# Kernel optimization log

Measured on AMD Instinct MI355X. Metric: run time of the kernel, lower is better.

Reference implementation:

```python
import jax, jax.numpy as jnp
import numpy as np

N, E, F_IN, DIM, HEADS = 16384, 262144, 128, 64, 4
HID = DIM * HEADS  # 256
NEG = 0.2


def _lin(k, fan_in, fan_out):
    kw, kb = jax.random.split(k)
    s = 1.0 / np.sqrt(fan_in)
    return (jax.random.uniform(kw, (fan_in, fan_out), jnp.float32, -s, s),
            jax.random.uniform(kb, (fan_out,), jnp.float32, -s, s))


def setup_inputs() -> dict:
    key = jax.random.key(0)
    ks = jax.random.split(key, 20)
    x = jax.random.normal(ks[0], (N, F_IN), jnp.float32)
    edge_index = jax.random.randint(ks[1], (2, E), 0, N, jnp.int32)
    Win, b_in = _lin(ks[2], F_IN, DIM)
    Wskip, bskip = _lin(ks[3], DIM, HID)
    # conv1: in=DIM, out per head=DIM, heads=HEADS, concat -> HID
    Wl1, _ = _lin(ks[4], DIM, HID)
    Wr1, _ = _lin(ks[5], DIM, HID)
    att1 = jax.random.normal(ks[6], (HEADS, DIM), jnp.float32) * 0.1
    b1 = jnp.zeros((HID,), jnp.float32)
    # conv2: in=HID, out=HID, heads=1, concat=False
    Wl2, _ = _lin(ks[7], HID, HID)
    Wr2, _ = _lin(ks[8], HID, HID)
    att2 = jax.random.normal(ks[9], (1, HID), jnp.float32) * 0.1
    b2 = jnp.zeros((HID,), jnp.float32)
    # conv3: in=HID, out=HID, heads=1, concat=False
    Wl3, _ = _lin(ks[10], HID, HID)
    Wr3, _ = _lin(ks[11], HID, HID)
    att3 = jax.random.normal(ks[12], (1, HID), jnp.float32) * 0.1
    b3 = jnp.zeros((HID,), jnp.float32)
    Wm1, bm1 = _lin(ks[13], HID, DIM)
    Wm2, bm2 = _lin(ks[14], DIM, DIM)
    Wm3, bm3 = _lin(ks[15], DIM, 1)
    return dict(x=x, edge_index=edge_index, Win=Win, b_in=b_in,
                Wskip=Wskip, bskip=bskip,
                Wl1=Wl1, Wr1=Wr1, att1=att1, b1=b1,
                Wl2=Wl2, Wr2=Wr2, att2=att2, b2=b2,
                Wl3=Wl3, Wr3=Wr3, att3=att3, b3=b3,
                Wm1=Wm1, bm1=bm1, Wm2=Wm2, bm2=bm2, Wm3=Wm3, bm3=bm3)


def gatv2(x, src, dst, Wl, Wr, att, b, concat):
    # PyG GATv2Conv: x_l = lin_l(x)[src], x_r = lin_r(x)[dst]
    n = x.shape[0]
    H, D = att.shape
    xl = (x @ Wl).reshape(n, H, D)
    xr = (x @ Wr).reshape(n, H, D)
    e = jax.nn.leaky_relu(xl[src] + xr[dst], NEG)          # [E, H, D]
    logits = jnp.einsum('ehd,hd->eh', e, att)              # [E, H]
    m = jax.ops.segment_max(logits, dst, num_segments=n)   # per-dst softmax
    alpha = jnp.exp(logits - m[dst])
    denom = jax.ops.segment_sum(alpha, dst, num_segments=n)
    alpha = alpha / denom[dst]
    out = jax.ops.segment_sum(alpha[:, :, None] * xl[src], dst, num_segments=n)
    out = out.reshape(n, H * D) if concat else out.mean(axis=1)
    return out + b


def reference(x, edge_index, Win, b_in, Wskip, bskip,
              Wl1, Wr1, att1, b1, Wl2, Wr2, att2, b2,
              Wl3, Wr3, att3, b3, Wm1, bm1, Wm2, bm2, Wm3, bm3):
    n = x.shape[0]
    # add self loops (GATv2Conv default add_self_loops=True)
    loop = jnp.arange(n, dtype=edge_index.dtype)
    src = jnp.concatenate([edge_index[0], loop])
    dst = jnp.concatenate([edge_index[1], loop])

    h = jax.nn.relu(x @ Win + b_in)                         # [N, DIM]
    out1 = jax.nn.relu(gatv2(h, src, dst, Wl1, Wr1, att1, b1, True))
    out1 = out1 + (h @ Wskip + bskip)                       # [N, HID]
    out2 = jax.nn.relu(gatv2(out1, src, dst, Wl2, Wr2, att2, b2, False))
    out2 = out2 + out1
    out3 = jax.nn.relu(gatv2(out2, src, dst, Wl3, Wr3, att3, b3, False))
    out3 = out3 + out2
    out = jax.nn.relu(out3 @ Wm1 + bm1)
    out = jax.nn.relu(out @ Wm2 + bm2)
    out = out @ Wm3 + bm3                                   # [N, 1]
    return out.reshape(-1)
```

## Files before the change

### kernel.cpp

```cpp
#include <hip/hip_runtime.h>
#include <cstdint>
#include <cstddef>

#define N_NODES 16384
#define E_EDGES 262144
#define FIN     128
#define DIM     64
#define HID     256
#define NEG     0.2f

typedef _Float16 h8 __attribute__((ext_vector_type(8)));
typedef _Float16 h4 __attribute__((ext_vector_type(4)));
typedef _Float16 h2 __attribute__((ext_vector_type(2)));
typedef float    f32x4 __attribute__((ext_vector_type(4)));
typedef float    f32x2 __attribute__((ext_vector_type(2)));

__global__ __launch_bounds__(256) void zero_cnt_kernel(int4* __restrict__ cnt) {
    cnt[blockIdx.x * 256 + threadIdx.x] = make_int4(0, 0, 0, 0);
}

__global__ __launch_bounds__(256) void hist_kernel(const int* __restrict__ dst,
                                                   int* __restrict__ cnt) {
    int i = blockIdx.x * 256 + threadIdx.x;
    if (i < E_EDGES) atomicAdd(&cnt[dst[i]], 1);
}

__global__ __launch_bounds__(256) void csr_scan_kernel(const int* __restrict__ cnt,
                                                       int* __restrict__ offs,
                                                       int* __restrict__ cursor) {
    __shared__ int wsum[4];
    int tid = threadIdx.x, lane = tid & 63, w = tid >> 6;
    int base = tid * 64;
    const int4* c4 = (const int4*)(cnt + base);
    int4 v[16];
    int s = 0;
#pragma unroll
    for (int i = 0; i < 16; ++i) {
        v[i] = c4[i];
        s += v[i].x + v[i].y + v[i].z + v[i].w;
    }
    int scan = s;
#pragma unroll
    for (int off = 1; off < 64; off <<= 1) {
        int t = __shfl_up(scan, off);
        if (lane >= off) scan += t;
    }
    if (lane == 63) wsum[w] = scan;
    __syncthreads();
    int wbase = 0;
#pragma unroll
    for (int i = 0; i < 4; ++i) if (i < w) wbase += wsum[i];
    int run = wbase + (scan - s);
#pragma unroll
    for (int i = 0; i < 16; ++i) {
        int4 o;
        o.x = run;
        o.y = o.x + v[i].x;
        o.z = o.y + v[i].y;
        o.w = o.z + v[i].z;
        *(int4*)(offs + base + 4 * i) = o;
        *(int4*)(cursor + base + 4 * i) = o;
        run = o.w + v[i].w;
    }
    if (tid == 255) offs[N_NODES] = run;
}

__global__ __launch_bounds__(256) void scatter_kernel(const int* __restrict__ src,
                                                      const int* __restrict__ dst,
                                                      int* __restrict__ cursor,
                                                      int* __restrict__ esrc) {
    int i = blockIdx.x * 256 + threadIdx.x;
    if (i < E_EDGES) {
        int p = atomicAdd(&cursor[dst[i]], 1);
        esrc[p] = src[i];
    }
}

struct PackJob { const float* W; _Float16* dst; int Ksrc, Nsrc, NT, colOff; };
struct PackJobs { PackJob j[10]; };

__global__ __launch_bounds__(256) void pack_all_kernel(PackJobs jobs) {
    PackJob jb = jobs.j[blockIdx.y];
    int i = blockIdx.x * 256 + threadIdx.x;
    if (i < jb.Ksrc * jb.Nsrc) {
        int k = i / jb.Nsrc, n = i % jb.Nsrc;
        jb.dst[((size_t)(k >> 3) * jb.NT + jb.colOff + n) * 8 + (k & 7)] = (_Float16)jb.W[i];
    }
}

template<int K, bool RELU, bool O16, bool IN32>
__global__ __launch_bounds__(64) void mfma_n64_kernel(const void* __restrict__ Av,
                                                      const _Float16* __restrict__ Wp,
                                                      const float* __restrict__ bias,
                                                      void* __restrict__ outv) {
    int lane = threadIdx.x;
    int rowBase = blockIdx.x * 64;
    int l15 = lane & 15, l4 = lane >> 4;

    f32x4 acc[4][4] = {};
#pragma unroll
    for (int ks = 0; ks < K / 32; ++ks) {
        h8 af[4], bf[4];
#pragma unroll
        for (int mi = 0; mi < 4; ++mi) {
            if constexpr (IN32) {
                const float* ap = (const float*)Av + (size_t)(rowBase + mi * 16 + l15) * K + ks * 32 + l4 * 8;
                float4 a0 = *(const float4*)ap;
                float4 a1 = *(const float4*)(ap + 4);
                h8 v;
                v[0] = (_Float16)a0.x; v[1] = (_Float16)a0.y;
                v[2] = (_Float16)a0.z; v[3] = (_Float16)a0.w;
                v[4] = (_Float16)a1.x; v[5] = (_Float16)a1.y;
                v[6] = (_Float16)a1.z; v[7] = (_Float16)a1.w;
                af[mi] = v;
            } else {
                af[mi] = *(const h8*)((const _Float16*)Av + (size_t)(rowBase + mi * 16 + l15) * K + ks * 32 + l4 * 8);
            }
        }
#pragma unroll
        for (int ni = 0; ni < 4; ++ni)
            bf[ni] = *(const h8*)(Wp + ((size_t)(ks * 4 + l4) * 64 + ni * 16 + l15) * 8);
#pragma unroll
        for (int mi = 0; mi < 4; ++mi)
#pragma unroll
            for (int ni = 0; ni < 4; ++ni)
                acc[mi][ni] = __builtin_amdgcn_mfma_f32_16x16x32_f16(af[mi], bf[ni], acc[mi][ni], 0, 0, 0);
    }
#pragma unroll
    for (int mi = 0; mi < 4; ++mi)
#pragma unroll
        for (int ni = 0; ni < 4; ++ni) {
            int c = ni * 16 + l15;
            float bv = bias[c];
#pragma unroll
            for (int q = 0; q < 4; ++q) {
                int r = rowBase + mi * 16 + l4 * 4 + q;
                float v = acc[mi][ni][q] + bv;
                if (RELU) v = fmaxf(v, 0.f);
                if constexpr (O16) ((_Float16*)outv)[(size_t)r * 64 + c] = (_Float16)v;
                else               ((float*)outv)[(size_t)r * 64 + c] = v;
            }
        }
}

template<int K>
__global__ __launch_bounds__(256) void mfma_gemm_kernel(const _Float16* __restrict__ A,
                                                        const _Float16* __restrict__ Wp,
                                                        int NT,
                                                        _Float16* __restrict__ o16a,
                                                        _Float16* __restrict__ o16b,
                                                        float* __restrict__ o32,
                                                        const float* __restrict__ bias) {
    int tid = threadIdx.x;
    int lane = tid & 63, wid = tid >> 6;
    int wm = wid >> 1, wn = wid & 1;
    int rowBase = blockIdx.x * 128 + wm * 64;
    int colBase = blockIdx.y * 128 + wn * 64;
    int l15 = lane & 15, l4 = lane >> 4;

    f32x4 acc[4][4] = {};
#pragma unroll
    for (int ks = 0; ks < K / 32; ++ks) {
        h8 af[4], bf[4];
#pragma unroll
        for (int mi = 0; mi < 4; ++mi)
            af[mi] = *(const h8*)(A + (size_t)(rowBase + mi * 16 + l15) * K + ks * 32 + l4 * 8);
#pragma unroll
        for (int ni = 0; ni < 4; ++ni)
            bf[ni] = *(const h8*)(Wp + ((size_t)(ks * 4 + l4) * NT + colBase + ni * 16 + l15) * 8);
#pragma unroll
        for (int mi = 0; mi < 4; ++mi)
#pragma unroll
            for (int ni = 0; ni < 4; ++ni)
                acc[mi][ni] = __builtin_amdgcn_mfma_f32_16x16x32_f16(af[mi], bf[ni], acc[mi][ni], 0, 0, 0);
    }

    int seg = colBase >> 8;
    int cbase = colBase & 255;
    if (o32 != nullptr && seg == 2) {
#pragma unroll
        for (int mi = 0; mi < 4; ++mi)
#pragma unroll
            for (int ni = 0; ni < 4; ++ni) {
                int c = cbase + ni * 16 + l15;
                float bv = bias[c];
#pragma unroll
                for (int q = 0; q < 4; ++q) {
                    int r = rowBase + mi * 16 + l4 * 4 + q;
                    o32[(size_t)r * 256 + c] = acc[mi][ni][q] + bv;
                }
            }
    } else {
        _Float16* o = (seg == 0) ? o16a : o16b;
#pragma unroll
        for (int mi = 0; mi < 4; ++mi)
#pragma unroll
            for (int ni = 0; ni < 4; ++ni) {
                int c = cbase + ni * 16 + l15;
#pragma unroll
                for (int q = 0; q < 4; ++q) {
                    int r = rowBase + mi * 16 + l4 * 4 + q;
                    o[(size_t)r * 256 + c] = (_Float16)acc[mi][ni][q];
                }
            }
    }
}

template<int H, int OMODE>
__global__ __launch_bounds__(256) void gat_agg_kernel(const _Float16* __restrict__ xl,
                                                      const _Float16* __restrict__ xr,
                                                      const float* __restrict__ att,
                                                      const float* __restrict__ bias,
                                                      const float* __restrict__ resid,
                                                      const int* __restrict__ offs,
                                                      const int* __restrict__ esrc,
                                                      float* __restrict__ out,
                                                      _Float16* __restrict__ out16) {
    int tid = threadIdx.x;
    int wid = tid >> 6;
    int lane = tid & 63;
    int node = blockIdx.x * 4 + wid;
    int g  = lane >> 4;
    int li = lane & 15;

    h2 xrv[8];
    {
        const h8* xp = (const h8*)(xr + ((size_t)node << 8) + (li << 4));
        h8 a0 = xp[0], a1 = xp[1];
#pragma unroll
        for (int i = 0; i < 4; ++i) { xrv[i][0] = a0[2 * i]; xrv[i][1] = a0[2 * i + 1]; }
#pragma unroll
        for (int i = 0; i < 4; ++i) { xrv[4 + i][0] = a1[2 * i]; xrv[4 + i][1] = a1[2 * i + 1]; }
    }
    h2 attv[8];
    {
        const float4* ap = (const float4*)(att + (li << 4));
#pragma unroll
        for (int i = 0; i < 4; ++i) {
            float4 a = ap[i];
            attv[2 * i][0] = (_Float16)a.x; attv[2 * i][1] = (_Float16)a.y;
            attv[2 * i + 1][0] = (_Float16)a.z; attv[2 * i + 1][1] = (_Float16)a.w;
        }
    }
    const h2 negc = { (_Float16)NEG, (_Float16)NEG };

    float m = -1e30f, s = 0.f;
    f32x2 acc2[8];
#pragma unroll
    for (int i = 0; i < 8; ++i) acc2[i] = (f32x2){0.f, 0.f};

    int e0 = offs[node];
    int total = offs[node + 1] - e0 + 1;

    auto gather = [&](int srcn, h2* hv) {
        const h8* xp = (const h8*)(xl + ((size_t)srcn << 8) + (li << 4));
        h8 a0 = xp[0], a1 = xp[1];
#pragma unroll
        for (int i = 0; i < 4; ++i) { hv[i][0] = a0[2 * i]; hv[i][1] = a0[2 * i + 1]; }
#pragma unroll
        for (int i = 0; i < 4; ++i) { hv[4 + i][0] = a1[2 * i]; hv[4 + i][1] = a1[2 * i + 1]; }
    };
    auto logit = [&](const h2* hv) -> float {
        float part = 0.f;
#pragma unroll
        for (int i = 0; i < 8; ++i) {
            h2 sum = hv[i] + xrv[i];
            h2 lr = __builtin_elementwise_max(sum, sum * negc);
            part = __builtin_amdgcn_fdot2(lr, attv[i], part, false);
        }
        part += __shfl_xor(part, 1);
        part += __shfl_xor(part, 2);
        if constexpr (H == 1) {
            part += __shfl_xor(part, 4);
            part += __shfl_xor(part, 8);
        }
        return part;
    };

    int vi = g;
    for (; vi + 4 < total; vi += 8) {
        int sA = (vi == 0) ? node : esrc[e0 + vi - 1];
        int sB = esrc[e0 + vi + 3];
        h2 hA[8], hB[8];
        gather(sA, hA);
        gather(sB, hB);
        float lpA = logit(hA);
        float lpB = logit(hB);
        float mn = fmaxf(m, fmaxf(lpA, lpB));
        float c  = __expf(m - mn);
        float pA = __expf(lpA - mn);
        float pB = __expf(lpB - mn);
        s = s * c + pA + pB;
#pragma unroll
        for (int i = 0; i < 8; ++i) {
            f32x2 t = acc2[i] * c;
            t[0] = fmaf(pA, (float)hA[i][0], t[0]);
            t[1] = fmaf(pA, (float)hA[i][1], t[1]);
            t[0] = fmaf(pB, (float)hB[i][0], t[0]);
            t[1] = fmaf(pB, (float)hB[i][1], t[1]);
            acc2[i] = t;
        }
        m = mn;
    }
    for (; vi < total; vi += 4) {
        int srcn = (vi == 0) ? node : esrc[e0 + vi - 1];
        h2 hA[8];
        gather(srcn, hA);
        float lp = logit(hA);
        float mn = fmaxf(m, lp);
        float c = __expf(m - mn);
        float p = __expf(lp - mn);
        s = s * c + p;
#pragma unroll
        for (int i = 0; i < 8; ++i) {
            f32x2 t = acc2[i] * c;
            t[0] = fmaf(p, (float)hA[i][0], t[0]);
            t[1] = fmaf(p, (float)hA[i][1], t[1]);
            acc2[i] = t;
        }
        m = mn;
    }

#pragma unroll
    for (int mask = 16; mask <= 32; mask <<= 1) {
        float m2 = __shfl_xor(m, mask);
        float s2 = __shfl_xor(s, mask);
        float M = fmaxf(m, m2);
        float c1 = __expf(m - M);
        float c2 = __expf(m2 - M);
        s = s * c1 + s2 * c2;
#pragma unroll
        for (int i = 0; i < 8; ++i) {
            float ax = __shfl_xor(acc2[i][0], mask);
            float ay = __shfl_xor(acc2[i][1], mask);
            acc2[i][0] = acc2[i][0] * c1 + ax * c2;
            acc2[i][1] = acc2[i][1] * c1 + ay * c2;
        }
        m = M;
    }

    float inv = 1.f / s;
    float a0, a1v, a2, a3;
    if (g == 0)      { a0 = acc2[0][0]; a1v = acc2[0][1]; a2 = acc2[1][0]; a3 = acc2[1][1]; }
    else if (g == 1) { a0 = acc2[2][0]; a1v = acc2[2][1]; a2 = acc2[3][0]; a3 = acc2[3][1]; }
    else if (g == 2) { a0 = acc2[4][0]; a1v = acc2[4][1]; a2 = acc2[5][0]; a3 = acc2[5][1]; }
    else             { a0 = acc2[6][0]; a1v = acc2[6][1]; a2 = acc2[7][0]; a3 = acc2[7][1]; }
    int dbase = (li << 4) + (g << 2);
    float4 bv = *(const float4*)(bias + dbase);
    float4 rv = *(const float4*)(resid + ((size_t)node << 8) + dbase);
    float o0 = fmaxf(a0 * inv + bv.x, 0.f) + rv.x;
    float o1 = fmaxf(a1v * inv + bv.y, 0.f) + rv.y;
    float o2 = fmaxf(a2 * inv + bv.z, 0.f) + rv.z;
    float o3 = fmaxf(a3 * inv + bv.w, 0.f) + rv.w;
    if constexpr (OMODE != 2) {
        float4 ov = make_float4(o0, o1, o2, o3);
        *(float4*)(out + ((size_t)node << 8) + dbase) = ov;
    }
    if constexpr (OMODE != 0) {
        h4 hv;
        hv[0] = (_Float16)o0; hv[1] = (_Float16)o1;
        hv[2] = (_Float16)o2; hv[3] = (_Float16)o3;
        *(h4*)(out16 + ((size_t)node << 8) + dbase) = hv;
    }
}

__global__ __launch_bounds__(64) void mlp_head_kernel(const _Float16* __restrict__ A,
                                                      const _Float16* __restrict__ Wm1p,
                                                      const float* __restrict__ bm1,
                                                      const _Float16* __restrict__ Wm2p,
                                                      const float* __restrict__ bm2,
                                                      const float* __restrict__ Wm3,
                                                      const float* __restrict__ bm3,
                                                      float* __restrict__ out) {
    __shared__ _Float16 t1s[64][72];
    int lane = threadIdx.x;
    int rowBase = blockIdx.x * 64;
    int l15 = lane & 15, l4 = lane >> 4;

    f32x4 acc[4][4] = {};
#pragma unroll
    for (int ks = 0; ks < 8; ++ks) {
        h8 af[4], bf[4];
#pragma unroll
        for (int mi = 0; mi < 4; ++mi)
            af[mi] = *(const h8*)(A + (size_t)(rowBase + mi * 16 + l15) * 256 + ks * 32 + l4 * 8);
#pragma unroll
        for (int ni = 0; ni < 4; ++ni)
            bf[ni] = *(const h8*)(Wm1p + ((size_t)(ks * 4 + l4) * 64 + ni * 16 + l15) * 8);
#pragma unroll
        for (int mi = 0; mi < 4; ++mi)
#pragma unroll
            for (int ni = 0; ni < 4; ++ni)
                acc[mi][ni] = __builtin_amdgcn_mfma_f32_16x16x32_f16(af[mi], bf[ni], acc[mi][ni], 0, 0, 0);
    }
#pragma unroll
    for (int mi = 0; mi < 4; ++mi)
#pragma unroll
        for (int ni = 0; ni < 4; ++ni) {
            int c = ni * 16 + l15;
            float bv = bm1[c];
#pragma unroll
            for (int q = 0; q < 4; ++q)
                t1s[mi * 16 + l4 * 4 + q][c] = (_Float16)fmaxf(acc[mi][ni][q] + bv, 0.f);
        }

    f32x4 acc2[4][4] = {};
#pragma unroll
    for (int ks = 0; ks < 2; ++ks) {
        h8 af[4], bf[4];
#pragma unroll
        for (int mi = 0; mi < 4; ++mi)
            af[mi] = *(const h8*)&t1s[mi * 16 + l15][ks * 32 + l4 * 8];
#pragma unroll
        for (int ni = 0; ni < 4; ++ni)
            bf[ni] = *(const h8*)(Wm2p + ((size_t)(ks * 4 + l4) * 64 + ni * 16 + l15) * 8);
#pragma unroll
        for (int mi = 0; mi < 4; ++mi)
#pragma unroll
            for (int ni = 0; ni < 4; ++ni)
                acc2[mi][ni] = __builtin_amdgcn_mfma_f32_16x16x32_f16(af[mi], bf[ni], acc2[mi][ni], 0, 0, 0);
    }

    float b3 = bm3[0];
    float b2v[4], w3v[4];
#pragma unroll
    for (int ni = 0; ni < 4; ++ni) {
        b2v[ni] = bm2[ni * 16 + l15];
        w3v[ni] = Wm3[ni * 16 + l15];
    }
#pragma unroll
    for (int mi = 0; mi < 4; ++mi)
#pragma unroll
        for (int q = 0; q < 4; ++q) {
            float part = 0.f;
#pragma unroll
            for (int ni = 0; ni < 4; ++ni)
                part += fmaxf(acc2[mi][ni][q] + b2v[ni], 0.f) * w3v[ni];
            part += __shfl_xor(part, 1);
            part += __shfl_xor(part, 2);
            part += __shfl_xor(part, 4);
            part += __shfl_xor(part, 8);
            if (l15 == 0)
                out[rowBase + mi * 16 + l4 * 4 + q] = part + b3;
        }
}

extern "C" void kernel_launch(void* const* d_in, const int* in_sizes, int n_in,
                              void* d_out, int out_size, void* d_ws, size_t ws_size,
                              hipStream_t stream) {
    const float* x     = (const float*)d_in[0];
    const int*   ei    = (const int*)d_in[1];
    const float* Win   = (const float*)d_in[2];
    const float* b_in  = (const float*)d_in[3];
    const float* Wskip = (const float*)d_in[4];
    const float* bskip = (const float*)d_in[5];
    const float* Wl1   = (const float*)d_in[6];
    const float* Wr1   = (const float*)d_in[7];
    const float* att1  = (const float*)d_in[8];
    const float* b1    = (const float*)d_in[9];
    const float* Wl2   = (const float*)d_in[10];
    const float* Wr2   = (const float*)d_in[11];
    const float* att2  = (const float*)d_in[12];
    const float* b2    = (const float*)d_in[13];
    const float* Wl3   = (const float*)d_in[14];
    const float* Wr3   = (const float*)d_in[15];
    const float* att3  = (const float*)d_in[16];
    const float* b3    = (const float*)d_in[17];
    const float* Wm1   = (const float*)d_in[18];
    const float* bm1   = (const float*)d_in[19];
    const float* Wm2   = (const float*)d_in[20];
    const float* bm2   = (const float*)d_in[21];
    const float* Wm3   = (const float*)d_in[22];
    const float* bm3   = (const float*)d_in[23];

    char* p = (char*)d_ws;
    auto alloc = [&](size_t bytes) { char* r = p; p += (bytes + 255) & ~(size_t)255; return r; };
    const size_t NN = N_NODES;
    float*    skip = (float*)alloc(NN * 256 * 4);
    float*    out1 = (float*)alloc(NN * 256 * 4);
    _Float16* o116 = (_Float16*)alloc(NN * 256 * 2);
    _Float16* o216 = (_Float16*)alloc(NN * 256 * 2);
    _Float16* o316 = o116;
    _Float16* h16  = (_Float16*)alloc(NN * 64 * 2);
    _Float16* xl16 = (_Float16*)alloc(NN * 256 * 2);
    _Float16* xr16 = (_Float16*)alloc(NN * 256 * 2);
    _Float16* Wp1  = (_Float16*)alloc((size_t)64 * 768 * 2);
    _Float16* Wp2  = (_Float16*)alloc((size_t)256 * 512 * 2);
    _Float16* Wp3  = (_Float16*)alloc((size_t)256 * 512 * 2);
    _Float16* Winp = (_Float16*)alloc((size_t)128 * 64 * 2);
    _Float16* Wm1p = (_Float16*)alloc((size_t)256 * 64 * 2);
    _Float16* Wm2p = (_Float16*)alloc((size_t)64 * 64 * 2);
    int* cnt    = (int*)alloc(N_NODES * 4);
    int* offs   = (int*)alloc((N_NODES + 1) * 4);
    int* cursor = (int*)alloc(N_NODES * 4);
    int* esrc   = (int*)alloc(E_EDGES * 4);

    const int* src = ei;
    const int* dst = ei + E_EDGES;

    zero_cnt_kernel<<<N_NODES / 1024, 256, 0, stream>>>((int4*)cnt);
    hist_kernel<<<E_EDGES / 256, 256, 0, stream>>>(dst, cnt);
    csr_scan_kernel<<<1, 256, 0, stream>>>(cnt, offs, cursor);
    scatter_kernel<<<E_EDGES / 256, 256, 0, stream>>>(src, dst, cursor, esrc);

    PackJobs jobs = {{
        { Wl1,   Wp1,  64,  256, 768, 0   },
        { Wr1,   Wp1,  64,  256, 768, 256 },
        { Wskip, Wp1,  64,  256, 768, 512 },
        { Wl2,   Wp2,  256, 256, 512, 0   },
        { Wr2,   Wp2,  256, 256, 512, 256 },
        { Wl3,   Wp3,  256, 256, 512, 0   },
        { Wr3,   Wp3,  256, 256, 512, 256 },
        { Win,   Winp, 128, 64,  64,  0   },
        { Wm1,   Wm1p, 256, 64,  64,  0   },
        { Wm2,   Wm2p, 64,  64,  64,  0   },
    }};
    pack_all_kernel<<<dim3(256, 10), 256, 0, stream>>>(jobs);

    mfma_n64_kernel<128, true, true, true><<<N_NODES / 64, 64, 0, stream>>>(x, Winp, b_in, h16);

    mfma_gemm_kernel<64><<<dim3(128, 6), 256, 0, stream>>>(h16, Wp1, 768, xl16, xr16, skip, bskip);
    gat_agg_kernel<4, 1><<<N_NODES / 4, 256, 0, stream>>>(xl16, xr16, att1, b1, skip, offs, esrc, out1, o116);

    mfma_gemm_kernel<256><<<dim3(128, 4), 256, 0, stream>>>(o116, Wp2, 512, xl16, xr16, nullptr, nullptr);
    gat_agg_kernel<1, 1><<<N_NODES / 4, 256, 0, stream>>>(xl16, xr16, att2, b2, out1, offs, esrc, skip , o216);

    mfma_gemm_kernel<256><<<dim3(128, 4), 256, 0, stream>>>(o216, Wp3, 512, xl16, xr16, nullptr, nullptr);
    gat_agg_kernel<1, 2><<<N_NODES / 4, 256, 0, stream>>>(xl16, xr16, att3, b3, skip , offs, esrc, nullptr, o316);

    mlp_head_kernel<<<N_NODES / 64, 64, 0, stream>>>(o316, Wm1p, bm1, Wm2p, bm2, Wm3, bm3, (float*)d_out);
}
```

Baseline: 198.7 us.

## Fold count zeroing into pack kernel, unroll GAT gather 4-wide, split MLP head across waves

Removes the separate zero_cnt launch by adding an extra grid row to the weight-pack kernel that clears the histogram counts. The GAT aggregation loop now processes four neighbours per iteration instead of two, giving more outstanding gathers for memory-level parallelism. The bias and residual loads are hoisted ahead of the loop so their latency overlaps it. The MLP head now uses 256-thread blocks with each wave handling 16 rows, which lowers register use per wave and raises occupancy, at the cost of more register pressure in the aggregation kernel.

Result: slower. 210.3 us (+5.8%).

```diff
diff --git a/kernel.cpp b/kernel.cpp
--- a/kernel.cpp
+++ b/kernel.cpp
@@ -14,10 +14,6 @@
 typedef _Float16 h2 __attribute__((ext_vector_type(2)));
 typedef float    f32x4 __attribute__((ext_vector_type(4)));
 typedef float    f32x2 __attribute__((ext_vector_type(2)));
-
-__global__ __launch_bounds__(256) void zero_cnt_kernel(int4* __restrict__ cnt) {
-    cnt[blockIdx.x * 256 + threadIdx.x] = make_int4(0, 0, 0, 0);
-}
 
 __global__ __launch_bounds__(256) void hist_kernel(const int* __restrict__ dst,
                                                    int* __restrict__ cnt) {
@@ -79,9 +75,13 @@
 struct PackJob { const float* W; _Float16* dst; int Ksrc, Nsrc, NT, colOff; };
 struct PackJobs { PackJob j[10]; };
 
-__global__ __launch_bounds__(256) void pack_all_kernel(PackJobs jobs) {
+__global__ __launch_bounds__(256) void pack_all_kernel(PackJobs jobs, int* __restrict__ cnt) {
+    int i = blockIdx.x * 256 + threadIdx.x;
+    if (blockIdx.y == 10) {
+        if (i < N_NODES) cnt[i] = 0;
+        return;
+    }
     PackJob jb = jobs.j[blockIdx.y];
-    int i = blockIdx.x * 256 + threadIdx.x;
     if (i < jb.Ksrc * jb.Nsrc) {
         int k = i / jb.Nsrc, n = i % jb.Nsrc;
         jb.dst[((size_t)(k >> 3) * jb.NT + jb.colOff + n) * 8 + (k & 7)] = (_Float16)jb.W[i];
@@ -244,6 +244,10 @@
     }
     const h2 negc = { (_Float16)NEG, (_Float16)NEG };
 
+    int dbase = (li << 4) + (g << 2);
+    float4 bv = *(const float4*)(bias + dbase);
+    float4 rv = *(const float4*)(resid + ((size_t)node << 8) + dbase);
+
     float m = -1e30f, s = 0.f;
     f32x2 acc2[8];
 #pragma unroll
@@ -278,19 +282,27 @@
     };
 
     int vi = g;
-    for (; vi + 4 < total; vi += 8) {
+    for (; vi + 12 < total; vi += 16) {
         int sA = (vi == 0) ? node : esrc[e0 + vi - 1];
         int sB = esrc[e0 + vi + 3];
-        h2 hA[8], hB[8];
+        int sC = esrc[e0 + vi + 7];
+        int sD = esrc[e0 + vi + 11];
+        h2 hA[8], hB[8], hC[8], hD[8];
         gather(sA, hA);
         gather(sB, hB);
+        gather(sC, hC);
+        gather(sD, hD);
         float lpA = logit(hA);
         float lpB = logit(hB);
-        float mn = fmaxf(m, fmaxf(lpA, lpB));
+        float lpC = logit(hC);
+        float lpD = logit(hD);
+        float mn = fmaxf(m, fmaxf(fmaxf(lpA, lpB), fmaxf(lpC, lpD)));
         float c  = __expf(m - mn);
         float pA = __expf(lpA - mn);
         float pB = __expf(lpB - mn);
-        s = s * c + pA + pB;
+        float pC = __expf(lpC - mn);
+        float pD = __expf(lpD - mn);
+        s = s * c + ((pA + pB) + (pC + pD));
 #pragma unroll
         for (int i = 0; i < 8; ++i) {
             f32x2 t = acc2[i] * c;
@@ -298,6 +310,10 @@
             t[1] = fmaf(pA, (float)hA[i][1], t[1]);
             t[0] = fmaf(pB, (float)hB[i][0], t[0]);
             t[1] = fmaf(pB, (float)hB[i][1], t[1]);
+            t[0] = fmaf(pC, (float)hC[i][0], t[0]);
+            t[1] = fmaf(pC, (float)hC[i][1], t[1]);
+            t[0] = fmaf(pD, (float)hD[i][0], t[0]);
+            t[1] = fmaf(pD, (float)hD[i][1], t[1]);
             acc2[i] = t;
         }
         m = mn;
@@ -345,9 +361,6 @@
     else if (g == 1) { a0 = acc2[2][0]; a1v = acc2[2][1]; a2 = acc2[3][0]; a3 = acc2[3][1]; }
     else if (g == 2) { a0 = acc2[4][0]; a1v = acc2[4][1]; a2 = acc2[5][0]; a3 = acc2[5][1]; }
     else             { a0 = acc2[6][0]; a1v = acc2[6][1]; a2 = acc2[7][0]; a3 = acc2[7][1]; }
-    int dbase = (li << 4) + (g << 2);
-    float4 bv = *(const float4*)(bias + dbase);
-    float4 rv = *(const float4*)(resid + ((size_t)node << 8) + dbase);
     float o0 = fmaxf(a0 * inv + bv.x, 0.f) + rv.x;
     float o1 = fmaxf(a1v * inv + bv.y, 0.f) + rv.y;
     float o2 = fmaxf(a2 * inv + bv.z, 0.f) + rv.z;
@@ -364,61 +377,52 @@
     }
 }
 
-__global__ __launch_bounds__(64) void mlp_head_kernel(const _Float16* __restrict__ A,
-                                                      const _Float16* __restrict__ Wm1p,
-                                                      const float* __restrict__ bm1,
-                                                      const _Float16* __restrict__ Wm2p,
-                                                      const float* __restrict__ bm2,
-                                                      const float* __restrict__ Wm3,
-                                                      const float* __restrict__ bm3,
-                                                      float* __restrict__ out) {
-    __shared__ _Float16 t1s[64][72];
-    int lane = threadIdx.x;
-    int rowBase = blockIdx.x * 64;
+__global__ __launch_bounds__(256) void mlp_head_kernel(const _Float16* __restrict__ A,
+                                                       const _Float16* __restrict__ Wm1p,
+                                                       const float* __restrict__ bm1,
+                                                       const _Float16* __restrict__ Wm2p,
+                                                       const float* __restrict__ bm2,
+                                                       const float* __restrict__ Wm3,
+                                                       const float* __restrict__ bm3,
+                                                       float* __restrict__ out) {
+    __shared__ _Float16 t1s[4][16][72];
+    int tid = threadIdx.x;
+    int lane = tid & 63, wid = tid >> 6;
+    int rowBase = blockIdx.x * 64 + wid * 16;
     int l15 = lane & 15, l4 = lane >> 4;
 
-    f32x4 acc[4][4] = {};
+    f32x4 acc[4] = {};
 #pragma unroll
     for (int ks = 0; ks < 8; ++ks) {
-        h8 af[4], bf[4];
-#pragma unroll
-        for (int mi = 0; mi < 4; ++mi)
-            af[mi] = *(const h8*)(A + (size_t)(rowBase + mi * 16 + l15) * 256 + ks * 32 + l4 * 8);
+        h8 af = *(const h8*)(A + (size_t)(rowBase + l15) * 256 + ks * 32 + l4 * 8);
+        h8 bf[4];
 #pragma unroll
         for (int ni = 0; ni < 4; ++ni)
             bf[ni] = *(const h8*)(Wm1p + ((size_t)(ks * 4 + l4) * 64 + ni * 16 + l15) * 8);
 #pragma unroll
-        for (int mi = 0; mi < 4; ++mi)
-#pragma unroll
-            for (int ni = 0; ni < 4; ++ni)
-                acc[mi][ni] = __builtin_amdgcn_mfma_f32_16x16x32_f16(af[mi], bf[ni], acc[mi][ni], 0, 0, 0);
-    }
-#pragma unroll
-    for (int mi = 0; mi < 4; ++mi)
-#pragma unroll
-        for (int ni = 0; ni < 4; ++ni) {
-            int c = ni * 16 + l15;
-            float bv = bm1[c];
-#pragma unroll
-            for (int q = 0; q < 4; ++q)
-                t1s[mi * 16 + l4 * 4 + q][c] = (_Float16)fmaxf(acc[mi][ni][q] + bv, 0.f);
-        }
-
-    f32x4 acc2[4][4] = {};
+        for (int ni = 0; ni < 4; ++ni)
+            acc[ni] = __builtin_amdgcn_mfma_f32_16x16x32_f16(af, bf[ni], acc[ni], 0, 0, 0);
+    }
+#pragma unroll
+    for (int ni = 0; ni < 4; ++ni) {
+        int c = ni * 16 + l15;
+        float bv = bm1[c];
+#pragma unroll
+        for (int q = 0; q < 4; ++q)
+            t1s[wid][l4 * 4 + q][c] = (_Float16)fmaxf(acc[ni][q] + bv, 0.f);
+    }
+
+    f32x4 acc2[4] = {};
 #pragma unroll
     for (int ks = 0; ks < 2; ++ks) {
-        h8 af[4], bf[4];
-#pragma unroll
-        for (int mi = 0; mi < 4; ++mi)
-            af[mi] = *(const h8*)&t1s[mi * 16 + l15][ks * 32 + l4 * 8];
+        h8 af = *(const h8*)&t1s[wid][l15][ks * 32 + l4 * 8];
+        h8 bf[4];
 #pragma unroll
         for (int ni = 0; ni < 4; ++ni)
             bf[ni] = *(const h8*)(Wm2p + ((size_t)(ks * 4 + l4) * 64 + ni * 16 + l15) * 8);
 #pragma unroll
-        for (int mi = 0; mi < 4; ++mi)
-#pragma unroll
-            for (int ni = 0; ni < 4; ++ni)
-                acc2[mi][ni] = __builtin_amdgcn_mfma_f32_16x16x32_f16(af[mi], bf[ni], acc2[mi][ni], 0, 0, 0);
+        for (int ni = 0; ni < 4; ++ni)
+            acc2[ni] = __builtin_amdgcn_mfma_f32_16x16x32_f16(af, bf[ni], acc2[ni], 0, 0, 0);
     }
 
     float b3 = bm3[0];
@@ -429,20 +433,18 @@
         w3v[ni] = Wm3[ni * 16 + l15];
     }
 #pragma unroll
-    for (int mi = 0; mi < 4; ++mi)
-#pragma unroll
-        for (int q = 0; q < 4; ++q) {
-            float part = 0.f;
-#pragma unroll
-            for (int ni = 0; ni < 4; ++ni)
-                part += fmaxf(acc2[mi][ni][q] + b2v[ni], 0.f) * w3v[ni];
-            part += __shfl_xor(part, 1);
-            part += __shfl_xor(part, 2);
-            part += __shfl_xor(part, 4);
-            part += __shfl_xor(part, 8);
-            if (l15 == 0)
-                out[rowBase + mi * 16 + l4 * 4 + q] = part + b3;
-        }
+    for (int q = 0; q < 4; ++q) {
+        float part = 0.f;
+#pragma unroll
+        for (int ni = 0; ni < 4; ++ni)
+            part += fmaxf(acc2[ni][q] + b2v[ni], 0.f) * w3v[ni];
+        part += __shfl_xor(part, 1);
+        part += __shfl_xor(part, 2);
+        part += __shfl_xor(part, 4);
+        part += __shfl_xor(part, 8);
+        if (l15 == 0)
+            out[rowBase + l4 * 4 + q] = part + b3;
+    }
 }
 
 extern "C" void kernel_launch(void* const* d_in, const int* in_sizes, int n_in,
@@ -498,11 +500,6 @@
     const int* src = ei;
     const int* dst = ei + E_EDGES;
 
-    zero_cnt_kernel<<<N_NODES / 1024, 256, 0, stream>>>((int4*)cnt);
-    hist_kernel<<<E_EDGES / 256, 256, 0, stream>>>(dst, cnt);
-    csr_scan_kernel<<<1, 256, 0, stream>>>(cnt, offs, cursor);
-    scatter_kernel<<<E_EDGES / 256, 256, 0, stream>>>(src, dst, cursor, esrc);
-
     PackJobs jobs = {{
         { Wl1,   Wp1,  64,  256, 768, 0   },
         { Wr1,   Wp1,  64,  256, 768, 256 },
@@ -515,7 +512,11 @@
         { Wm1,   Wm1p, 256, 64,  64,  0   },
         { Wm2,   Wm2p, 64,  64,  64,  0   },
     }};
-    pack_all_kernel<<<dim3(256, 10), 256, 0, stream>>>(jobs);
+    pack_all_kernel<<<dim3(256, 11), 256, 0, stream>>>(jobs, cnt);
+
+    hist_kernel<<<E_EDGES / 256, 256, 0, stream>>>(dst, cnt);
+    csr_scan_kernel<<<1, 256, 0, stream>>>(cnt, offs, cursor);
+    scatter_kernel<<<E_EDGES / 256, 256, 0, stream>>>(src, dst, cursor, esrc);
 
     mfma_n64_kernel<128, true, true, true><<<N_NODES / 64, 64, 0, stream>>>(x, Winp, b_in, h16);
 
@@ -528,5 +529,5 @@
     mfma_gemm_kernel<256><<<dim3(128, 4), 256, 0, stream>>>(o216, Wp3, 512, xl16, xr16, nullptr, nullptr);
     gat_agg_kernel<1, 2><<<N_NODES / 4, 256, 0, stream>>>(xl16, xr16, att3, b3, skip , offs, esrc, nullptr, o316);
 
-    mlp_head_kernel<<<N_NODES / 64, 64, 0, stream>>>(o316, Wm1p, bm1, Wm2p, bm2, Wm3, bm3, (float*)d_out);
-}
+    mlp_head_kernel<<<N_NODES / 64, 256, 0, stream>>>(o316, Wm1p, bm1, Wm2p, bm2, Wm3, bm3, (float*)d_out);
+}
```
